# Optimization experiments

Measured on AMD Instinct MI355X. Metric: run time of the kernel, lower is better.

The kernel has to match this reference:

```python
import jax, jax.numpy as jnp
import numpy as np

N = 100_000      # total nodes in batched graph
NE = 800_000     # total edges
G = 1_000        # number of graphs in batch
V_DIM = 128      # node feat dim (== H_DIM, required by GRUCell usage)
E_DIM = 64       # edge feat dim
H_DIM = 128      # hidden dim
K_HEAD = 4       # multi-scale interaction heads


def _leaky(x):
    return jnp.where(x >= 0, x, 0.1 * x)


def _gru_cell(x, h, Wih, Whh, bih, bhh):
    # torch nn.GRUCell math; Wih/Whh stored as [in, 3*h] with (r,z,n) chunk order
    gi = x @ Wih + bih
    gh = h @ Whh + bhh
    ir, iz, inn = jnp.split(gi, 3, axis=-1)
    hr, hz, hn = jnp.split(gh, 3, axis=-1)
    r = jax.nn.sigmoid(ir + hr)
    z = jax.nn.sigmoid(iz + hz)
    n = jnp.tanh(inn + r * hn)
    return (1.0 - z) * n + z * h


def setup_inputs() -> dict:
    key = jax.random.key(0)
    ks = iter(jax.random.split(key, 48))
    def rn(shape, scale=0.05):
        return (jax.random.normal(next(ks), shape) * scale).astype(jnp.float32)
    inp = {}
    inp["v"] = rn((N, V_DIM), 1.0)
    inp["e"] = rn((NE, E_DIM), 1.0)
    inp["s"] = rn((G, V_DIM), 1.0)
    inp["edge_src"] = jax.random.randint(next(ks), (NE,), 0, N)
    inp["edge_dst"] = jax.random.randint(next(ks), (NE,), 0, N)
    inp["node_graph"] = jnp.repeat(jnp.arange(G), N // G)  # sorted segment ids
    # top-level linears (stored [in, out])
    inp["A_w"] = rn((V_DIM, H_DIM)); inp["A_b"] = rn((H_DIM,))
    inp["mA_w"] = rn((K_HEAD, V_DIM, H_DIM)); inp["mA_b"] = rn((K_HEAD, H_DIM))
    inp["mB_w"] = rn((K_HEAD, V_DIM, H_DIM)); inp["mB_b"] = rn((K_HEAD, H_DIM))
    inp["mC_w"] = rn((K_HEAD, H_DIM)); inp["mC_b"] = rn((K_HEAD,))
    inp["mD_w"] = rn((K_HEAD, V_DIM, H_DIM)); inp["mD_b"] = rn((K_HEAD, H_DIM))
    inp["B_w"] = rn((H_DIM * K_HEAD, H_DIM)); inp["B_b"] = rn((H_DIM,))
    inp["C_w"] = rn((V_DIM, H_DIM)); inp["C_b"] = rn((H_DIM,))
    inp["K_w"] = rn((E_DIM, H_DIM)); inp["K_b"] = rn((H_DIM,))
    inp["E_w"] = rn((H_DIM + V_DIM, H_DIM)); inp["E_b"] = rn((H_DIM,))
    for pfx in ("gm", "gs"):
        inp[pfx + "_A_w"] = rn((H_DIM, H_DIM)); inp[pfx + "_A_b"] = rn((H_DIM,))
        inp[pfx + "_B_w"] = rn((H_DIM, H_DIM)); inp[pfx + "_B_b"] = rn((H_DIM,))
        inp[pfx + "_Wih"] = rn((H_DIM, 3 * H_DIM)); inp[pfx + "_Whh"] = rn((H_DIM, 3 * H_DIM))
        inp[pfx + "_bih"] = rn((3 * H_DIM,)); inp[pfx + "_bhh"] = rn((3 * H_DIM,))
    return inp


def reference(v, e, s, edge_src, edge_dst, node_graph,
              A_w, A_b, mA_w, mA_b, mB_w, mB_b, mC_w, mC_b, mD_w, mD_b,
              B_w, B_b, C_w, C_b, K_w, K_b, E_w, E_b,
              gm_A_w, gm_A_b, gm_B_w, gm_B_b, gm_Wih, gm_Whh, gm_bih, gm_bhh,
              gs_A_w, gs_A_b, gs_B_w, gs_B_b, gs_Wih, gs_Whh, gs_bih, gs_bhh):
    # super -> super
    s2s = jnp.tanh(s @ A_w + A_b)                                       # [G,H]
    # multi-head node->super attention pooling (Multi_scale_interaction)
    d_node = jnp.tanh(jnp.einsum('nv,kvh->knh', v, mA_w) + mA_b[:, None, :])     # [K,N,H]
    d_super = jnp.tanh(jnp.einsum('gv,kvh->kgh', s, mB_w) + mB_b[:, None, :])    # [K,G,H]
    a = jnp.einsum('knh,kh->nk', d_node * d_super[:, node_graph, :], mC_w) + mC_b[None, :]  # [N,K]
    a_max = jax.ops.segment_max(a, node_graph, num_segments=G, indices_are_sorted=True)
    a_exp = jnp.exp(a - a_max[node_graph])
    denom = jax.ops.segment_sum(a_exp, node_graph, num_segments=G, indices_are_sorted=True)
    attn = a_exp / denom[node_graph]                                    # per-graph softmax, [N,K]
    d_v = jnp.einsum('nv,kvh->nkh', v, mD_w) + mD_b[None, :, :]         # [N,K,H]
    pooled = jax.ops.segment_sum(d_v * attn[:, :, None], node_graph, num_segments=G,
                                 indices_are_sorted=True)               # [G,K,H]
    m2s = jnp.tanh(pooled.reshape(G, K_HEAD * H_DIM) @ B_w + B_b)       # [G,H]
    # super -> node broadcast
    s2m = jnp.tanh(s @ C_w + C_b)[node_graph]                           # [N,H]
    # edge-wise message: leaky_relu(K(e) * v_src) summed into destination node
    ve = _leaky((e @ K_w + K_b) * v[edge_src])                          # [E,H]
    sve = jax.ops.segment_sum(ve, edge_dst, num_segments=N)             # [N,H]
    m2m = _leaky(jnp.concatenate([sve, v], axis=1) @ E_w + E_b)         # [N,H]
    # adaptive GRU gate: node update
    z_m = jax.nn.sigmoid(m2m @ gm_A_w + gm_A_b + s2m @ gm_B_w + gm_B_b)
    h_m = z_m * s2m + (1.0 - z_m) * m2m
    update_v = _gru_cell(v, h_m, gm_Wih, gm_Whh, gm_bih, gm_bhh)
    # adaptive GRU gate: supernode update
    z_s = jax.nn.sigmoid(s2s @ gs_A_w + gs_A_b + m2s @ gs_B_w + gs_B_b)
    h_s = z_s * m2s + (1.0 - z_s) * s2s
    update_s = _gru_cell(s, h_s, gs_Wih, gs_Whh, gs_bih, gs_bhh)
    return (update_v, update_s)
```

## Files before the change

### kernel.cpp

```cpp
#include <hip/hip_runtime.h>

#define NN   100000
#define NEDG 800000
#define NG   1000
#define HD   128
#define EDIM 64

typedef unsigned short u16;
typedef __bf16 bf16x8 __attribute__((ext_vector_type(8)));
typedef float f32x4 __attribute__((ext_vector_type(4)));
typedef u16 u16x8 __attribute__((ext_vector_type(8)));

#define MFMA16(a, b, c) __builtin_amdgcn_mfma_f32_16x16x32_bf16(a, b, c, 0, 0, 0)

#define WS_E    0
#define WS_GA   4096
#define WS_WIH  6144
#define WS_WHH  12288
#define WS_MA0  18432
#define WS_KW   26624
#define WS_LANES 27648

#define BF(base, NTT, ks, nt, lane) \
    (*(const bf16x8*)(wsw + (size_t)((base) + (((ks) * (NTT) + (nt)) * 64 + (lane))) * 8))

__device__ __forceinline__ float sigmoidf_(float x) { return 1.0f / (1.0f + __expf(-x)); }
__device__ __forceinline__ float tanhf_(float x) {
    float ax = fabsf(x);
    float e  = __expf(-2.0f * ax);
    float t  = (1.0f - e) / (1.0f + e);
    return copysignf(t, x);
}
__device__ __forceinline__ float leaky_(float x) { return x >= 0.f ? x : 0.1f * x; }
__device__ __forceinline__ u16 f2bf(float x) {
    union { float f; unsigned u; } c; c.f = x;
    unsigned r = c.u + 0x7FFF + ((c.u >> 16) & 1);
    return (u16)(r >> 16);
}
__device__ __forceinline__ float bfbits2f(unsigned hw) {
    union { unsigned u; float f; } c; c.u = hw << 16; return c.f;
}

__device__ __forceinline__ void stg4(u16* lds, int P, int r, int c0, float4 v4) {
    int byteoff = (c0 << 1) ^ ((r & 7) << 4);
    u16* p = lds + r * P + (byteoff >> 1);
    p[0] = f2bf(v4.x); p[1] = f2bf(v4.y); p[2] = f2bf(v4.z); p[3] = f2bf(v4.w);
}
__device__ __forceinline__ void stg1(u16* lds, int P, int r, int c, u16 val) {
    int byteoff = (c << 1) ^ ((r & 7) << 4);
    lds[r * P + (byteoff >> 1)] = val;
}
__device__ __forceinline__ bf16x8 ldA(const u16* lds, int P, int r, int ks, int hi) {
    int byteoff = (ks * 64 + (hi << 4)) ^ ((r & 7) << 4);
    return *(const bf16x8*)(lds + r * P + (byteoff >> 1));
}

__global__ __launch_bounds__(256) void wconv(
    const float* __restrict__ E_w, const float* __restrict__ gmA_w,
    const float* __restrict__ Wih, const float* __restrict__ Whh,
    const float* __restrict__ mA_w, const float* __restrict__ K_w,
    u16* __restrict__ dst)
{
    int t = blockIdx.x * 256 + threadIdx.x;
    if (t >= WS_LANES) return;
    const float* W; int N; int local;
    if (t < 4096)       { W = E_w;  N = 128; local = t; }
    else if (t < 6144)  { W = gmA_w; N = 128; local = t - 4096; }
    else if (t < 12288) { W = Wih;  N = 384; local = t - 6144; }
    else if (t < 18432) { W = Whh;  N = 384; local = t - 12288; }
    else if (t < 26624) { int k = (t - 18432) >> 11; W = mA_w + k * 128 * 128; N = 128; local = (t - 18432) & 2047; }
    else                { W = K_w;  N = 128; local = t - 26624; }
    int lane = local & 63;
    int fid  = local >> 6;
    int NT = N >> 4;
    int ks = fid / NT, nt = fid - ks * NT;
    int krow = ks * 32 + ((lane >> 4) << 3);
    int col  = nt * 16 + (lane & 15);
    u16* d = dst + (size_t)t * 8;
    #pragma unroll
    for (int j = 0; j < 8; j++) d[j] = f2bf(W[(size_t)(krow + j) * N + col]);
}

__global__ __launch_bounds__(256) void k_hist(const int* __restrict__ edst, int* __restrict__ cnt) {
    int i = blockIdx.x * 256 + threadIdx.x;
    if (i < NEDG) atomicAdd(&cnt[edst[i]], 1);
}

__global__ __launch_bounds__(256) void k_scan1(const int* __restrict__ cnt,
                                               int* __restrict__ excl, int* __restrict__ bsum) {
    __shared__ int sd[256];
    int t = threadIdx.x, b = blockIdx.x;
    int base = b * 1024 + t * 4;
    int v0 = (base + 0 < NN) ? cnt[base + 0] : 0;
    int v1 = (base + 1 < NN) ? cnt[base + 1] : 0;
    int v2 = (base + 2 < NN) ? cnt[base + 2] : 0;
    int v3 = (base + 3 < NN) ? cnt[base + 3] : 0;
    int s = v0 + v1 + v2 + v3;
    sd[t] = s;
    __syncthreads();
    for (int off = 1; off < 256; off <<= 1) {
        int x = (t >= off) ? sd[t - off] : 0;
        __syncthreads();
        sd[t] += x;
        __syncthreads();
    }
    int incl = sd[t];
    int ex = incl - s;
    if (base + 0 < NN) excl[base + 0] = ex;
    if (base + 1 < NN) excl[base + 1] = ex + v0;
    if (base + 2 < NN) excl[base + 2] = ex + v0 + v1;
    if (base + 3 < NN) excl[base + 3] = ex + v0 + v1 + v2;
    if (t == 255) bsum[b] = incl;
}

#define NSCB 98
__global__ void k_scan2(int* __restrict__ bsum) {
    if (threadIdx.x == 0 && blockIdx.x == 0) {
        int run = 0;
        for (int i = 0; i < NSCB; i++) { int t = bsum[i]; bsum[i] = run; run += t; }
    }
}

__global__ __launch_bounds__(256) void k_scan3(const int* __restrict__ excl,
                                               const int* __restrict__ bsum,
                                               int* __restrict__ start, int* __restrict__ rowptr) {
    int i = blockIdx.x * 256 + threadIdx.x;
    if (i < NN) {
        int sv = excl[i] + bsum[i >> 10];
        start[i] = sv;
        rowptr[i] = sv;
    }
    if (i == NN) rowptr[NN] = NEDG;
}

__global__ __launch_bounds__(256) void k_scatter(const int* __restrict__ edst,
                                                 int* __restrict__ start,
                                                 int* __restrict__ perm,
                                                 int* __restrict__ outpos) {
    int i = blockIdx.x * 256 + threadIdx.x;
    if (i < NEDG) {
        int pos = atomicAdd(&start[edst[i]], 1);
        perm[pos] = i;
        outpos[i] = pos;
    }
}

__global__ __launch_bounds__(128) void k1_graph(
    const float* __restrict__ s,
    const float* __restrict__ A_w, const float* __restrict__ A_b,
    const float* __restrict__ mB_w, const float* __restrict__ mB_b,
    const float* __restrict__ mC_w,
    const float* __restrict__ C_w, const float* __restrict__ C_b,
    const float* __restrict__ gmB_w, const float* __restrict__ gmA_b, const float* __restrict__ gmB_b,
    float* __restrict__ s2s, float* __restrict__ wkg,
    float* __restrict__ s2m_tab, float* __restrict__ t2)
{
    __shared__ float sm[HD];
    __shared__ float sm2[HD];
    const int g = blockIdx.x, t = threadIdx.x;
    sm[t] = s[g * HD + t];
    __syncthreads();
    {
        float a = 0.f;
        #pragma unroll 8
        for (int i = 0; i < HD; i++) a = fmaf(sm[i], A_w[i * HD + t], a);
        s2s[g * HD + t] = tanhf_(a + A_b[t]);
    }
    for (int k = 0; k < 4; k++) {
        float a = 0.f;
        const float* W = mB_w + k * HD * HD;
        #pragma unroll 8
        for (int i = 0; i < HD; i++) a = fmaf(sm[i], W[i * HD + t], a);
        float d = tanhf_(a + mB_b[k * HD + t]);
        wkg[(k * NG + g) * HD + t] = d * mC_w[k * HD + t];
    }
    float s2m;
    {
        float a = 0.f;
        #pragma unroll 8
        for (int i = 0; i < HD; i++) a = fmaf(sm[i], C_w[i * HD + t], a);
        s2m = tanhf_(a + C_b[t]);
        s2m_tab[g * HD + t] = s2m;
    }
    sm2[t] = s2m;
    __syncthreads();
    {
        float a = 0.f;
        #pragma unroll 8
        for (int i = 0; i < HD; i++) a = fmaf(sm2[i], gmB_w[i * HD + t], a);
        t2[g * HD + t] = a + gmA_b[t] + gmB_b[t];
    }
}

__global__ __launch_bounds__(256) void k2_ascore(
    const float* __restrict__ v, const int* __restrict__ ngr,
    const u16* __restrict__ wsw,
    const float* __restrict__ mA_b, const float* __restrict__ mC_b,
    const float* __restrict__ wkg,
    float* __restrict__ aexp, float* __restrict__ denom)
{
    __shared__ u16 VT[64 * 128];
    const int tid = threadIdx.x;
    const int n0 = blockIdx.x * 64;
    #pragma unroll
    for (int l = 0; l < 8; l++) {
        int i = tid + 256 * l;
        int r = i >> 5, c0 = (i & 31) << 2;
        int node = n0 + r;
        float4 vv = (node < NN) ? *(const float4*)(v + (size_t)node * HD + c0)
                                : make_float4(0.f, 0.f, 0.f, 0.f);
        stg4(VT, 128, r, c0, vv);
    }
    __syncthreads();
    const int lane = tid & 63, w = tid >> 6;
    const int l15 = lane & 15, hi = lane >> 4;
    const int rbase = w * 16;
    bf16x8 av[4];
    #pragma unroll
    for (int ks = 0; ks < 4; ks++) av[ks] = ldA(VT, 128, rbase + l15, ks, hi);
    int gq[4], nodeq[4];
    #pragma unroll
    for (int q = 0; q < 4; q++) {
        int nd = n0 + rbase + hi * 4 + q;
        nodeq[q] = nd;
        gq[q] = ngr[min(nd, NN - 1)];
    }
    for (int k = 0; k < 4; k++) {
        float rs[4] = {0.f, 0.f, 0.f, 0.f};
        const float* bias = mA_b + k * HD;
        #pragma unroll
        for (int nt = 0; nt < 8; nt++) {
            f32x4 acc = {0.f, 0.f, 0.f, 0.f};
            #pragma unroll
            for (int ks = 0; ks < 4; ks++)
                acc = MFMA16(av[ks], BF(WS_MA0 + k * 2048, 8, ks, nt, lane), acc);
            int col = nt * 16 + l15;
            float bb = bias[col];
            #pragma unroll
            for (int q = 0; q < 4; q++)
                rs[q] += tanhf_(acc[q] + bb) * wkg[((size_t)k * NG + gq[q]) * HD + col];
        }
        #pragma unroll
        for (int q = 0; q < 4; q++) {
            float x = rs[q];
            x += __shfl_xor(x, 1); x += __shfl_xor(x, 2);
            x += __shfl_xor(x, 4); x += __shfl_xor(x, 8);
            if (l15 == 0 && nodeq[q] < NN) {
                float ev = __expf(x + mC_b[k]);
                aexp[(size_t)nodeq[q] * 4 + k] = ev;
                atomicAdd(&denom[gq[q] * 4 + k], ev);
            }
        }
    }
}

__global__ __launch_bounds__(256) void k3a_edge(
    const float* __restrict__ e, const float* __restrict__ v,
    const int* __restrict__ esrc, const int* __restrict__ outpos,
    const u16* __restrict__ wsw, const float* __restrict__ K_b,
    u16* __restrict__ vesrt)
{
    __shared__ u16 ET[64 * 64];
    __shared__ u16 OUT[64 * 128];
    __shared__ int posa[64];
    const int tid = threadIdx.x;
    const int e0 = blockIdx.x * 64;
    if (tid < 64) posa[tid] = outpos[e0 + tid];
    #pragma unroll
    for (int l = 0; l < 4; l++) {
        int i = tid + 256 * l;
        int r = i >> 4, c0 = (i & 15) << 2;
        float4 ev4 = *(const float4*)(e + (size_t)(e0 + r) * EDIM + c0);
        stg4(ET, 64, r, c0, ev4);
    }
    __syncthreads();
    const int lane = tid & 63, w = tid >> 6;
    const int l15 = lane & 15, hi = lane >> 4;
    const int rbase = w * 16;
    bf16x8 ae[2];
    #pragma unroll
    for (int ks = 0; ks < 2; ks++) ae[ks] = ldA(ET, 64, rbase + l15, ks, hi);
    int sq[4];
    #pragma unroll
    for (int q = 0; q < 4; q++) sq[q] = esrc[e0 + rbase + hi * 4 + q];
    #pragma unroll
    for (int nt = 0; nt < 8; nt++) {
        f32x4 acc = {0.f, 0.f, 0.f, 0.f};
        acc = MFMA16(ae[0], BF(WS_KW, 8, 0, nt, lane), acc);
        acc = MFMA16(ae[1], BF(WS_KW, 8, 1, nt, lane), acc);
        int col = nt * 16 + l15;
        float kb = K_b[col];
        #pragma unroll
        for (int q = 0; q < 4; q++) {
            float val = leaky_((acc[q] + kb) * v[(size_t)sq[q] * HD + col]);
            stg1(OUT, 128, rbase + hi * 4 + q, col, f2bf(val));
        }
    }
    __syncthreads();
    #pragma unroll
    for (int l = 0; l < 4; l++) {
        int i = tid + 256 * l;
        int r = i >> 4, seg = i & 15;
        int segp = seg ^ (r & 7);
        u16x8 val = *(const u16x8*)&OUT[r * 128 + segp * 8];
        *(u16x8*)(vesrt + (size_t)posa[r] * HD + ((segp ^ (r & 7)) * 8)) = val;
    }
}

__global__ __launch_bounds__(256) void k3b_segsum(
    const u16* __restrict__ vesrt, const int* __restrict__ rowptr,
    float* __restrict__ sve)
{
    const int wid = threadIdx.x >> 6, lane = threadIdx.x & 63;
    const int n = blockIdx.x * 4 + wid;
    if (n >= NN) return;
    const int r0 = rowptr[n], r1 = rowptr[n + 1];
    const unsigned* base = (const unsigned*)vesrt;
    float a0 = 0.f, a1 = 0.f;
    int r = r0;
    for (; r + 4 <= r1; r += 4) {
        unsigned x0 = base[(size_t)(r + 0) * 64 + lane];
        unsigned x1 = base[(size_t)(r + 1) * 64 + lane];
        unsigned x2 = base[(size_t)(r + 2) * 64 + lane];
        unsigned x3 = base[(size_t)(r + 3) * 64 + lane];
        a0 += bfbits2f(x0 & 0xffff) + bfbits2f(x1 & 0xffff) + bfbits2f(x2 & 0xffff) + bfbits2f(x3 & 0xffff);
        a1 += bfbits2f(x0 >> 16) + bfbits2f(x1 >> 16) + bfbits2f(x2 >> 16) + bfbits2f(x3 >> 16);
    }
    for (; r < r1; r++) {
        unsigned x = base[(size_t)r * 64 + lane];
        a0 += bfbits2f(x & 0xffff);
        a1 += bfbits2f(x >> 16);
    }
    *(float2*)(sve + (size_t)n * HD + lane * 2) = make_float2(a0, a1);
}

__global__ __launch_bounds__(256) void k3_edge_sorted(
    const float* __restrict__ e, const float* __restrict__ v,
    const int* __restrict__ esrc, const int* __restrict__ edst,
    const int* __restrict__ perm,
    const u16* __restrict__ wsw, const float* __restrict__ K_b,
    float* __restrict__ sve)
{
    __shared__ u16 ET[64 * 64];
    __shared__ int pid[64];
    const int tid = threadIdx.x;
    const int e0 = blockIdx.x * 64;
    if (tid < 64) pid[tid] = perm[e0 + tid];
    __syncthreads();
    #pragma unroll
    for (int l = 0; l < 4; l++) {
        int i = tid + 256 * l;
        int r = i >> 4, c0 = (i & 15) << 2;
        float4 ev4 = *(const float4*)(e + (size_t)pid[r] * EDIM + c0);
        stg4(ET, 64, r, c0, ev4);
    }
    __syncthreads();
    const int lane = tid & 63, w = tid >> 6;
    const int l15 = lane & 15, hi = lane >> 4;
    const int rbase = w * 16;
    bf16x8 ae[2];
    #pragma unroll
    for (int ks = 0; ks < 2; ks++) ae[ks] = ldA(ET, 64, rbase + l15, ks, hi);
    int sq[4], dq[4];
    #pragma unroll
    for (int q = 0; q < 4; q++) {
        int ei = pid[rbase + hi * 4 + q];
        sq[q] = esrc[ei]; dq[q] = edst[ei];
    }
    #pragma unroll
    for (int nt = 0; nt < 8; nt++) {
        f32x4 acc = {0.f, 0.f, 0.f, 0.f};
        acc = MFMA16(ae[0], BF(WS_KW, 8, 0, nt, lane), acc);
        acc = MFMA16(ae[1], BF(WS_KW, 8, 1, nt, lane), acc);
        int col = nt * 16 + l15;
        float kb = K_b[col];
        float vals[4];
        #pragma unroll
        for (int q = 0; q < 4; q++)
            vals[q] = leaky_((acc[q] + kb) * v[(size_t)sq[q] * HD + col]);
        float a = vals[0];
        #pragma unroll
        for (int q = 1; q < 4; q++) {
            if (dq[q] == dq[q - 1]) a += vals[q];
            else { atomicAdd(&sve[(size_t)dq[q - 1] * HD + col], a); a = vals[q]; }
        }
        atomicAdd(&sve[(size_t)dq[3] * HD + col], a);
    }
}

__global__ __launch_bounds__(256) void k3_edge_unsorted(
    const float* __restrict__ e, const float* __restrict__ v,
    const int* __restrict__ esrc, const int* __restrict__ edst,
    const u16* __restrict__ wsw, const float* __restrict__ K_b,
    float* __restrict__ sve)
{
    __shared__ u16 ET[64 * 64];
    const int tid = threadIdx.x;
    const int e0 = blockIdx.x * 64;
    #pragma unroll
    for (int l = 0; l < 4; l++) {
        int i = tid + 256 * l;
        int r = i >> 4, c0 = (i & 15) << 2;
        float4 ev4 = *(const float4*)(e + (size_t)(e0 + r) * EDIM + c0);
        stg4(ET, 64, r, c0, ev4);
    }
    __syncthreads();
    const int lane = tid & 63, w = tid >> 6;
    const int l15 = lane & 15, hi = lane >> 4;
    const int rbase = w * 16;
    bf16x8 ae[2];
    #pragma unroll
    for (int ks = 0; ks < 2; ks++) ae[ks] = ldA(ET, 64, rbase + l15, ks, hi);
    int sq[4], dq[4];
    #pragma unroll
    for (int q = 0; q < 4; q++) {
        int ei = e0 + rbase + hi * 4 + q;
        sq[q] = esrc[ei]; dq[q] = edst[ei];
    }
    #pragma unroll
    for (int nt = 0; nt < 8; nt++) {
        f32x4 acc = {0.f, 0.f, 0.f, 0.f};
        acc = MFMA16(ae[0], BF(WS_KW, 8, 0, nt, lane), acc);
        acc = MFMA16(ae[1], BF(WS_KW, 8, 1, nt, lane), acc);
        int col = nt * 16 + l15;
        float kb = K_b[col];
        #pragma unroll
        for (int q = 0; q < 4; q++) {
            float val = leaky_((acc[q] + kb) * v[(size_t)sq[q] * HD + col]);
            atomicAdd(&sve[(size_t)dq[q] * HD + col], val);
        }
    }
}

__global__ __launch_bounds__(256) void k4_vbar(
    const float* __restrict__ v, const int* __restrict__ ngr,
    const float* __restrict__ aexp, const float* __restrict__ denom,
    float* __restrict__ vbar)
{
    const int tid = threadIdx.x;
    const int d = tid & 127;
    const int hf = tid >> 7;
    const int n0 = blockIdx.x * 32 + hf * 16;
    int gcur = -1;
    float a0 = 0.f, a1 = 0.f, a2 = 0.f, a3 = 0.f;
    float4 rd = make_float4(0.f, 0.f, 0.f, 0.f);
    for (int nd = 0; nd < 16; nd++) {
        int n = n0 + nd;
        int g = ngr[n];
        if (g != gcur) {
            if (gcur >= 0) {
                atomicAdd(&vbar[(gcur * 4 + 0) * HD + d], a0);
                atomicAdd(&vbar[(gcur * 4 + 1) * HD + d], a1);
                atomicAdd(&vbar[(gcur * 4 + 2) * HD + d], a2);
                atomicAdd(&vbar[(gcur * 4 + 3) * HD + d], a3);
                a0 = a1 = a2 = a3 = 0.f;
            }
            float4 dn = *(const float4*)&denom[g * 4];
            rd = make_float4(1.f / dn.x, 1.f / dn.y, 1.f / dn.z, 1.f / dn.w);
            gcur = g;
        }
        float4 ae = *(const float4*)&aexp[n * 4];
        float vv = v[(size_t)n * HD + d];
        a0 = fmaf(ae.x * rd.x, vv, a0);
        a1 = fmaf(ae.y * rd.y, vv, a1);
        a2 = fmaf(ae.z * rd.z, vv, a2);
        a3 = fmaf(ae.w * rd.w, vv, a3);
    }
    atomicAdd(&vbar[(gcur * 4 + 0) * HD + d], a0);
    atomicAdd(&vbar[(gcur * 4 + 1) * HD + d], a1);
    atomicAdd(&vbar[(gcur * 4 + 2) * HD + d], a2);
    atomicAdd(&vbar[(gcur * 4 + 3) * HD + d], a3);
}

__global__ __launch_bounds__(128) void k5_super(
    const float* __restrict__ s, const float* __restrict__ vbar,
    const float* __restrict__ mD_w, const float* __restrict__ mD_b,
    const float* __restrict__ B_w, const float* __restrict__ B_b,
    const float* __restrict__ s2s,
    const float* __restrict__ gsA_w, const float* __restrict__ gsA_b,
    const float* __restrict__ gsB_w, const float* __restrict__ gsB_b,
    const float* __restrict__ gsWih, const float* __restrict__ gsWhh,
    const float* __restrict__ gsbih, const float* __restrict__ gsbhh,
    float* __restrict__ out_s)
{
    __shared__ float vb[4 * HD];
    __shared__ float p[4 * HD];
    __shared__ float m2s_l[HD];
    __shared__ float s2s_l[HD];
    __shared__ float hs_l[HD];
    __shared__ float srow[HD];
    const int g = blockIdx.x, t = threadIdx.x;
    #pragma unroll
    for (int l = 0; l < 4; l++) vb[t + HD * l] = vbar[(size_t)g * 4 * HD + t + HD * l];
    srow[t]  = s[g * HD + t];
    s2s_l[t] = s2s[g * HD + t];
    __syncthreads();
    for (int k = 0; k < 4; k++) {
        float a = 0.f;
        const float* W = mD_w + k * HD * HD;
        #pragma unroll 8
        for (int i = 0; i < HD; i++) a = fmaf(vb[k * HD + i], W[i * HD + t], a);
        p[k * HD + t] = a + mD_b[k * HD + t];
    }
    __syncthreads();
    float m2s;
    {
        float a = 0.f;
        #pragma unroll 8
        for (int j = 0; j < 4 * HD; j++) a = fmaf(p[j], B_w[j * HD + t], a);
        m2s = tanhf_(a + B_b[t]);
        m2s_l[t] = m2s;
    }
    __syncthreads();
    float hs;
    {
        float za = 0.f, zb = 0.f;
        #pragma unroll 8
        for (int i = 0; i < HD; i++) {
            za = fmaf(s2s_l[i], gsA_w[i * HD + t], za);
            zb = fmaf(m2s_l[i], gsB_w[i * HD + t], zb);
        }
        float z = sigmoidf_(za + gsA_b[t] + zb + gsB_b[t]);
        hs = z * m2s + (1.f - z) * s2s_l[t];
        hs_l[t] = hs;
    }
    __syncthreads();
    float gi0 = 0.f, gh0 = 0.f, gi1 = 0.f, gh1 = 0.f, gi2 = 0.f, gh2 = 0.f;
    #pragma unroll 4
    for (int i = 0; i < HD; i++) {
        float sv = srow[i], hv = hs_l[i];
        gi0 = fmaf(sv, gsWih[i * 384 + t], gi0);
        gh0 = fmaf(hv, gsWhh[i * 384 + t], gh0);
        gi1 = fmaf(sv, gsWih[i * 384 + 128 + t], gi1);
        gh1 = fmaf(hv, gsWhh[i * 384 + 128 + t], gh1);
        gi2 = fmaf(sv, gsWih[i * 384 + 256 + t], gi2);
        gh2 = fmaf(hv, gsWhh[i * 384 + 256 + t], gh2);
    }
    float r  = sigmoidf_(gi0 + gsbih[t] + gh0 + gsbhh[t]);
    float z2 = sigmoidf_(gi1 + gsbih[128 + t] + gh1 + gsbhh[128 + t]);
    float nn = tanhf_(gi2 + gsbih[256 + t] + r * (gh2 + gsbhh[256 + t]));
    out_s[g * HD + t] = (1.f - z2) * nn + z2 * hs;
}

__global__ __launch_bounds__(256) void k6_node(
    const float* __restrict__ v, const int* __restrict__ ngr,
    const float* __restrict__ sve, const u16* __restrict__ wsw,
    const float* __restrict__ E_b,
    const float* __restrict__ s2m_tab, const float* __restrict__ t2,
    const float* __restrict__ bih, const float* __restrict__ bhh,
    float* __restrict__ out_v)
{
    __shared__ u16 VT[64 * 128];
    __shared__ u16 ST[64 * 128];
    __shared__ u16 XT[64 * 128];
    const int tid = threadIdx.x;
    const int n0 = blockIdx.x * 64;
    #pragma unroll
    for (int l = 0; l < 8; l++) {
        int i = tid + 256 * l;
        int r = i >> 5, c0 = (i & 31) << 2;
        int node = n0 + r;
        float4 a = (node < NN) ? *(const float4*)(v   + (size_t)node * HD + c0) : make_float4(0.f, 0.f, 0.f, 0.f);
        float4 b = (node < NN) ? *(const float4*)(sve + (size_t)node * HD + c0) : make_float4(0.f, 0.f, 0.f, 0.f);
        stg4(VT, 128, r, c0, a);
        stg4(ST, 128, r, c0, b);
    }
    __syncthreads();
    const int lane = tid & 63, w = tid >> 6;
    const int l15 = lane & 15, hi = lane >> 4;
    const int rbase = w * 16;
    bf16x8 av[4], ax[4];
    #pragma unroll
    for (int ks = 0; ks < 4; ks++) {
        av[ks] = ldA(VT, 128, rbase + l15, ks, hi);
        ax[ks] = ldA(ST, 128, rbase + l15, ks, hi);
    }
    int gq[4], nodeq[4];
    #pragma unroll
    for (int q = 0; q < 4; q++) {
        int nd = n0 + rbase + hi * 4 + q;
        nodeq[q] = nd;
        gq[q] = ngr[min(nd, NN - 1)];
    }
    f32x4 hmf[8];
    #pragma unroll
    for (int nt = 0; nt < 8; nt++) {
        f32x4 acc = {0.f, 0.f, 0.f, 0.f};
        #pragma unroll
        for (int ks = 0; ks < 4; ks++) acc = MFMA16(ax[ks], BF(WS_E, 8, ks, nt, lane), acc);
        #pragma unroll
        for (int ks = 0; ks < 4; ks++) acc = MFMA16(av[ks], BF(WS_E, 8, 4 + ks, nt, lane), acc);
        int col = nt * 16 + l15;
        float eb = E_b[col];
        f32x4 m;
        #pragma unroll
        for (int q = 0; q < 4; q++) m[q] = leaky_(acc[q] + eb);
        hmf[nt] = m;
    }
    #pragma unroll
    for (int nt = 0; nt < 8; nt++) {
        int col = nt * 16 + l15;
        #pragma unroll
        for (int q = 0; q < 4; q++) stg1(ST, 128, rbase + hi * 4 + q, col, f2bf(hmf[nt][q]));
    }
    bf16x8 am[4];
    #pragma unroll
    for (int ks = 0; ks < 4; ks++) am[ks] = ldA(ST, 128, rbase + l15, ks, hi);
    #pragma unroll
    for (int nt = 0; nt < 8; nt++) {
        f32x4 acc = {0.f, 0.f, 0.f, 0.f};
        #pragma unroll
        for (int ks = 0; ks < 4; ks++) acc = MFMA16(am[ks], BF(WS_GA, 8, ks, nt, lane), acc);
        int col = nt * 16 + l15;
        #pragma unroll
        for (int q = 0; q < 4; q++) {
            int g = gq[q];
            float z  = sigmoidf_(acc[q] + t2[(size_t)g * HD + col]);
            float hm = z * s2m_tab[(size_t)g * HD + col] + (1.f - z) * hmf[nt][q];
            hmf[nt][q] = hm;
            stg1(XT, 128, rbase + hi * 4 + q, col, f2bf(hm));
        }
    }
    bf16x8 ah[4];
    #pragma unroll
    for (int ks = 0; ks < 4; ks++) ah[ks] = ldA(XT, 128, rbase + l15, ks, hi);
    #pragma unroll
    for (int nt = 0; nt < 8; nt++) {
        f32x4 air = {0.f,0.f,0.f,0.f}, aiz = {0.f,0.f,0.f,0.f}, ain = {0.f,0.f,0.f,0.f};
        f32x4 ahr = {0.f,0.f,0.f,0.f}, ahz = {0.f,0.f,0.f,0.f}, ahn = {0.f,0.f,0.f,0.f};
        #pragma unroll
        for (int ks = 0; ks < 4; ks++) {
            air = MFMA16(av[ks], BF(WS_WIH, 24, ks, nt,      lane), air);
            ahr = MFMA16(ah[ks], BF(WS_WHH, 24, ks, nt,      lane), ahr);
            aiz = MFMA16(av[ks], BF(WS_WIH, 24, ks, nt + 8,  lane), aiz);
            ahz = MFMA16(ah[ks], BF(WS_WHH, 24, ks, nt + 8,  lane), ahz);
            ain = MFMA16(av[ks], BF(WS_WIH, 24, ks, nt + 16, lane), ain);
            ahn = MFMA16(ah[ks], BF(WS_WHH, 24, ks, nt + 16, lane), ahn);
        }
        int col = nt * 16 + l15;
        float br  = bih[col] + bhh[col];
        float bz  = bih[HD + col] + bhh[HD + col];
        float bi3 = bih[2 * HD + col];
        float bh3 = bhh[2 * HD + col];
        #pragma unroll
        for (int q = 0; q < 4; q++) {
            float r   = sigmoidf_(air[q] + ahr[q] + br);
            float z   = sigmoidf_(aiz[q] + ahz[q] + bz);
            float nnv = tanhf_(ain[q] + bi3 + r * (ahn[q] + bh3));
            if (nodeq[q] < NN)
                out_v[(size_t)nodeq[q] * HD + col] = (1.f - z) * nnv + z * hmf[nt][q];
        }
    }
}

extern "C" void kernel_launch(void* const* d_in, const int* in_sizes, int n_in,
                              void* d_out, int out_size, void* d_ws, size_t ws_size,
                              hipStream_t stream)
{
    const float* v    = (const float*)d_in[0];
    const float* e    = (const float*)d_in[1];
    const float* s    = (const float*)d_in[2];
    const int*   esrc = (const int*)d_in[3];
    const int*   edst = (const int*)d_in[4];
    const int*   ngr  = (const int*)d_in[5];
    const float* A_w  = (const float*)d_in[6];
    const float* A_b  = (const float*)d_in[7];
    const float* mA_w = (const float*)d_in[8];
    const float* mA_b = (const float*)d_in[9];
    const float* mB_w = (const float*)d_in[10];
    const float* mB_b = (const float*)d_in[11];
    const float* mC_w = (const float*)d_in[12];
    const float* mC_b = (const float*)d_in[13];
    const float* mD_w = (const float*)d_in[14];
    const float* mD_b = (const float*)d_in[15];
    const float* B_w  = (const float*)d_in[16];
    const float* B_b  = (const float*)d_in[17];
    const float* C_w  = (const float*)d_in[18];
    const float* C_b  = (const float*)d_in[19];
    const float* K_w  = (const float*)d_in[20];
    const float* K_b  = (const float*)d_in[21];
    const float* E_w  = (const float*)d_in[22];
    const float* E_b  = (const float*)d_in[23];
    const float* gmA_w = (const float*)d_in[24];
    const float* gmA_b = (const float*)d_in[25];
    const float* gmB_w = (const float*)d_in[26];
    const float* gmB_b = (const float*)d_in[27];
    const float* gmWih = (const float*)d_in[28];
    const float* gmWhh = (const float*)d_in[29];
    const float* gmbih = (const float*)d_in[30];
    const float* gmbhh = (const float*)d_in[31];
    const float* gsA_w = (const float*)d_in[32];
    const float* gsA_b = (const float*)d_in[33];
    const float* gsB_w = (const float*)d_in[34];
    const float* gsB_b = (const float*)d_in[35];
    const float* gsWih = (const float*)d_in[36];
    const float* gsWhh = (const float*)d_in[37];
    const float* gsbih = (const float*)d_in[38];
    const float* gsbhh = (const float*)d_in[39];

    float* ws      = (float*)d_ws;
    float* sve     = ws;
    float* aexp    = sve + 12800000;
    float* denom   = aexp + 400000;
    float* wkg     = denom + 4000;
    float* s2s     = wkg + 512000;
    float* s2m_tab = s2s + 128000;
    float* t2      = s2m_tab + 128000;
    float* vbar    = t2 + 128000;
    u16*   wswz    = (u16*)(vbar + 512000);
    int*   isc     = (int*)(wswz + 221184);
    int*   cnt     = isc;
    int*   excl    = cnt + 100000;
    int*   bsum    = excl + 100000;
    int*   startp  = bsum + 128;
    int*   rowptr  = startp + 100000;
    int*   perm    = rowptr + 100032;
    int*   outpos  = perm + 800000;
    u16*   vesrt   = (u16*)(outpos + 800000);
    const size_t NEED_SORT = ((size_t)((int*)vesrt - (int*)d_ws)) * 4;
    const size_t NEED_FULL = NEED_SORT + (size_t)102400000 * 2;
    const bool do_sort = ws_size >= NEED_SORT;
    const bool do_full = ws_size >= NEED_FULL;

    hipMemsetAsync(denom, 0, (size_t)4000 * 4, stream);
    hipMemsetAsync(vbar, 0, (size_t)512000 * 4, stream);
    if (!do_full) hipMemsetAsync(sve, 0, (size_t)12800000 * 4, stream);

    float* out_v = (float*)d_out;
    float* out_s = out_v + (size_t)NN * HD;

    wconv<<<(WS_LANES + 255) / 256, 256, 0, stream>>>(E_w, gmA_w, gmWih, gmWhh, mA_w, K_w, wswz);
    k1_graph<<<NG, 128, 0, stream>>>(s, A_w, A_b, mB_w, mB_b, mC_w, C_w, C_b,
                                     gmB_w, gmA_b, gmB_b, s2s, wkg, s2m_tab, t2);
    if (do_sort) {
        hipMemsetAsync(cnt, 0, (size_t)100000 * 4, stream);
        k_hist<<<(NEDG + 255) / 256, 256, 0, stream>>>(edst, cnt);
        k_scan1<<<NSCB, 256, 0, stream>>>(cnt, excl, bsum);
        k_scan2<<<1, 64, 0, stream>>>(bsum);
        k_scan3<<<(NN + 256) / 256, 256, 0, stream>>>(excl, bsum, startp, rowptr);
        k_scatter<<<(NEDG + 255) / 256, 256, 0, stream>>>(edst, startp, perm, outpos);
    }
    k2_ascore<<<(NN + 63) / 64, 256, 0, stream>>>(v, ngr, wswz, mA_b, mC_b, wkg, aexp, denom);
    if (do_full) {
        k3a_edge<<<NEDG / 64, 256, 0, stream>>>(e, v, esrc, outpos, wswz, K_b, vesrt);
        k3b_segsum<<<(NN + 3) / 4, 256, 0, stream>>>(vesrt, rowptr, sve);
    } else if (do_sort) {
        k3_edge_sorted<<<NEDG / 64, 256, 0, stream>>>(e, v, esrc, edst, perm, wswz, K_b, sve);
    } else {
        k3_edge_unsorted<<<NEDG / 64, 256, 0, stream>>>(e, v, esrc, edst, wswz, K_b, sve);
    }
    k4_vbar<<<NN / 32, 256, 0, stream>>>(v, ngr, aexp, denom, vbar);
    k5_super<<<NG, 128, 0, stream>>>(s, vbar, mD_w, mD_b, B_w, B_b, s2s,
                                     gsA_w, gsA_b, gsB_w, gsB_b,
                                     gsWih, gsWhh, gsbih, gsbhh, out_s);
    k6_node<<<(NN + 63) / 64, 256, 0, stream>>>(v, ngr, sve, wswz, E_b, s2m_tab, t2,
                                                gmbih, gmbhh, out_v);
}
```

Before: 734.7 us.

## Swap MFMA operands to compute transposed tiles and drop LDS staging

The MFMA operands are swapped so each lane holds one node or edge row with 4 contiguous output columns. Inputs are loaded straight from global memory into bf16 fragments, and outputs are written as float4/u16x4 vectors. Shared-memory staging, the syncthreads barriers and the scalar LDS stores are removed. In the node kernel, the intermediate activations are redistributed between MFMA stages with cross-lane shuffles instead of an LDS round-trip. The trade-off is more shuffles and per-lane strided global reads of input rows that were previously coalesced through LDS.

```diff
diff --git a/kernel.cpp b/kernel.cpp
--- a/kernel.cpp
+++ b/kernel.cpp
@@ -9,7 +9,8 @@
 typedef unsigned short u16;
 typedef __bf16 bf16x8 __attribute__((ext_vector_type(8)));
 typedef float f32x4 __attribute__((ext_vector_type(4)));
-typedef u16 u16x8 __attribute__((ext_vector_type(8)));
+typedef u16 u16x4 __attribute__((ext_vector_type(4)));
+typedef unsigned u32x4 __attribute__((ext_vector_type(4)));
 
 #define MFMA16(a, b, c) __builtin_amdgcn_mfma_f32_16x16x32_bf16(a, b, c, 0, 0, 0)
 
@@ -40,15 +41,24 @@
 __device__ __forceinline__ float bfbits2f(unsigned hw) {
     union { unsigned u; float f; } c; c.u = hw << 16; return c.f;
 }
+__device__ __forceinline__ unsigned pack2bf(float lo, float hi) {
+    return (unsigned)f2bf(lo) | ((unsigned)f2bf(hi) << 16);
+}
+__device__ __forceinline__ bf16x8 mk8(const float* __restrict__ p) {
+    float4 a = *(const float4*)p;
+    float4 b = *(const float4*)(p + 4);
+    union { u32x4 u; bf16x8 v; } c;
+    c.u[0] = pack2bf(a.x, a.y);
+    c.u[1] = pack2bf(a.z, a.w);
+    c.u[2] = pack2bf(b.x, b.y);
+    c.u[3] = pack2bf(b.z, b.w);
+    return c.v;
+}
 
 __device__ __forceinline__ void stg4(u16* lds, int P, int r, int c0, float4 v4) {
     int byteoff = (c0 << 1) ^ ((r & 7) << 4);
     u16* p = lds + r * P + (byteoff >> 1);
     p[0] = f2bf(v4.x); p[1] = f2bf(v4.y); p[2] = f2bf(v4.z); p[3] = f2bf(v4.w);
-}
-__device__ __forceinline__ void stg1(u16* lds, int P, int r, int c, u16 val) {
-    int byteoff = (c << 1) ^ ((r & 7) << 4);
-    lds[r * P + (byteoff >> 1)] = val;
 }
 __device__ __forceinline__ bf16x8 ldA(const u16* lds, int P, int r, int ks, int hi) {
     int byteoff = (ks * 64 + (hi << 4)) ^ ((r & 7) << 4);
@@ -199,57 +209,37 @@
     const float* __restrict__ wkg,
     float* __restrict__ aexp, float* __restrict__ denom)
 {
-    __shared__ u16 VT[64 * 128];
     const int tid = threadIdx.x;
-    const int n0 = blockIdx.x * 64;
-    #pragma unroll
-    for (int l = 0; l < 8; l++) {
-        int i = tid + 256 * l;
-        int r = i >> 5, c0 = (i & 31) << 2;
-        int node = n0 + r;
-        float4 vv = (node < NN) ? *(const float4*)(v + (size_t)node * HD + c0)
-                                : make_float4(0.f, 0.f, 0.f, 0.f);
-        stg4(VT, 128, r, c0, vv);
-    }
-    __syncthreads();
     const int lane = tid & 63, w = tid >> 6;
-    const int l15 = lane & 15, hi = lane >> 4;
-    const int rbase = w * 16;
+    const int l15 = lane & 15, hi = lane >> 4, cb = hi * 4;
+    const int node = blockIdx.x * 64 + w * 16 + l15;
+    const int nodec = min(node, NN - 1);
+    const int g = ngr[nodec];
     bf16x8 av[4];
     #pragma unroll
-    for (int ks = 0; ks < 4; ks++) av[ks] = ldA(VT, 128, rbase + l15, ks, hi);
-    int gq[4], nodeq[4];
-    #pragma unroll
-    for (int q = 0; q < 4; q++) {
-        int nd = n0 + rbase + hi * 4 + q;
-        nodeq[q] = nd;
-        gq[q] = ngr[min(nd, NN - 1)];
-    }
+    for (int ks = 0; ks < 4; ks++) av[ks] = mk8(v + (size_t)nodec * HD + ks * 32 + hi * 8);
+    #pragma unroll
     for (int k = 0; k < 4; k++) {
-        float rs[4] = {0.f, 0.f, 0.f, 0.f};
+        float rs = 0.f;
         const float* bias = mA_b + k * HD;
+        const float* wrow = wkg + ((size_t)k * NG + g) * HD;
         #pragma unroll
         for (int nt = 0; nt < 8; nt++) {
             f32x4 acc = {0.f, 0.f, 0.f, 0.f};
             #pragma unroll
             for (int ks = 0; ks < 4; ks++)
-                acc = MFMA16(av[ks], BF(WS_MA0 + k * 2048, 8, ks, nt, lane), acc);
-            int col = nt * 16 + l15;
-            float bb = bias[col];
-            #pragma unroll
-            for (int q = 0; q < 4; q++)
-                rs[q] += tanhf_(acc[q] + bb) * wkg[((size_t)k * NG + gq[q]) * HD + col];
+                acc = MFMA16(BF(WS_MA0 + k * 2048, 8, ks, nt, lane), av[ks], acc);
+            float4 bb = *(const float4*)&bias[nt * 16 + cb];
+            float4 wk = *(const float4*)&wrow[nt * 16 + cb];
+            rs += tanhf_(acc[0] + bb.x) * wk.x + tanhf_(acc[1] + bb.y) * wk.y
+                + tanhf_(acc[2] + bb.z) * wk.z + tanhf_(acc[3] + bb.w) * wk.w;
         }
-        #pragma unroll
-        for (int q = 0; q < 4; q++) {
-            float x = rs[q];
-            x += __shfl_xor(x, 1); x += __shfl_xor(x, 2);
-            x += __shfl_xor(x, 4); x += __shfl_xor(x, 8);
-            if (l15 == 0 && nodeq[q] < NN) {
-                float ev = __expf(x + mC_b[k]);
-                aexp[(size_t)nodeq[q] * 4 + k] = ev;
-                atomicAdd(&denom[gq[q] * 4 + k], ev);
-            }
+        rs += __shfl_xor(rs, 16);
+        rs += __shfl_xor(rs, 32);
+        if (hi == 0 && node < NN) {
+            float ev = __expf(rs + mC_b[k]);
+            aexp[(size_t)node * 4 + k] = ev;
+            atomicAdd(&denom[g * 4 + k], ev);
         }
     }
 }
@@ -260,50 +250,29 @@
     const u16* __restrict__ wsw, const float* __restrict__ K_b,
     u16* __restrict__ vesrt)
 {
-    __shared__ u16 ET[64 * 64];
-    __shared__ u16 OUT[64 * 128];
-    __shared__ int posa[64];
     const int tid = threadIdx.x;
-    const int e0 = blockIdx.x * 64;
-    if (tid < 64) posa[tid] = outpos[e0 + tid];
-    #pragma unroll
-    for (int l = 0; l < 4; l++) {
-        int i = tid + 256 * l;
-        int r = i >> 4, c0 = (i & 15) << 2;
-        float4 ev4 = *(const float4*)(e + (size_t)(e0 + r) * EDIM + c0);
-        stg4(ET, 64, r, c0, ev4);
-    }
-    __syncthreads();
     const int lane = tid & 63, w = tid >> 6;
-    const int l15 = lane & 15, hi = lane >> 4;
-    const int rbase = w * 16;
-    bf16x8 ae[2];
-    #pragma unroll
-    for (int ks = 0; ks < 2; ks++) ae[ks] = ldA(ET, 64, rbase + l15, ks, hi);
-    int sq[4];
-    #pragma unroll
-    for (int q = 0; q < 4; q++) sq[q] = esrc[e0 + rbase + hi * 4 + q];
+    const int l15 = lane & 15, hi = lane >> 4, cb = hi * 4;
+    const int edge = blockIdx.x * 64 + w * 16 + l15;
+    const int sq = esrc[edge];
+    const int pos = outpos[edge];
+    bf16x8 ae0 = mk8(e + (size_t)edge * EDIM + hi * 8);
+    bf16x8 ae1 = mk8(e + (size_t)edge * EDIM + 32 + hi * 8);
+    const float* vrow = v + (size_t)sq * HD;
+    u16* drow = vesrt + (size_t)pos * HD;
     #pragma unroll
     for (int nt = 0; nt < 8; nt++) {
         f32x4 acc = {0.f, 0.f, 0.f, 0.f};
-        acc = MFMA16(ae[0], BF(WS_KW, 8, 0, nt, lane), acc);
-        acc = MFMA16(ae[1], BF(WS_KW, 8, 1, nt, lane), acc);
-        int col = nt * 16 + l15;
-        float kb = K_b[col];
-        #pragma unroll
-        for (int q = 0; q < 4; q++) {
-            float val = leaky_((acc[q] + kb) * v[(size_t)sq[q] * HD + col]);
-            stg1(OUT, 128, rbase + hi * 4 + q, col, f2bf(val));
-        }
-    }
-    __syncthreads();
-    #pragma unroll
-    for (int l = 0; l < 4; l++) {
-        int i = tid + 256 * l;
-        int r = i >> 4, seg = i & 15;
-        int segp = seg ^ (r & 7);
-        u16x8 val = *(const u16x8*)&OUT[r * 128 + segp * 8];
-        *(u16x8*)(vesrt + (size_t)posa[r] * HD + ((segp ^ (r & 7)) * 8)) = val;
+        acc = MFMA16(BF(WS_KW, 8, 0, nt, lane), ae0, acc);
+        acc = MFMA16(BF(WS_KW, 8, 1, nt, lane), ae1, acc);
+        float4 kb = *(const float4*)&K_b[nt * 16 + cb];
+        float4 vv = *(const float4*)&vrow[nt * 16 + cb];
+        u16x4 o;
+        o[0] = f2bf(leaky_((acc[0] + kb.x) * vv.x));
+        o[1] = f2bf(leaky_((acc[1] + kb.y) * vv.y));
+        o[2] = f2bf(leaky_((acc[2] + kb.z) * vv.z));
+        o[3] = f2bf(leaky_((acc[3] + kb.w) * vv.w));
+        *(u16x4*)(drow + nt * 16 + cb) = o;
     }
 }
 
@@ -550,106 +519,143 @@
     const float* __restrict__ bih, const float* __restrict__ bhh,
     float* __restrict__ out_v)
 {
-    __shared__ u16 VT[64 * 128];
-    __shared__ u16 ST[64 * 128];
-    __shared__ u16 XT[64 * 128];
     const int tid = threadIdx.x;
-    const int n0 = blockIdx.x * 64;
-    #pragma unroll
-    for (int l = 0; l < 8; l++) {
-        int i = tid + 256 * l;
-        int r = i >> 5, c0 = (i & 31) << 2;
-        int node = n0 + r;
-        float4 a = (node < NN) ? *(const float4*)(v   + (size_t)node * HD + c0) : make_float4(0.f, 0.f, 0.f, 0.f);
-        float4 b = (node < NN) ? *(const float4*)(sve + (size_t)node * HD + c0) : make_float4(0.f, 0.f, 0.f, 0.f);
-        stg4(VT, 128, r, c0, a);
-        stg4(ST, 128, r, c0, b);
-    }
-    __syncthreads();
     const int lane = tid & 63, w = tid >> 6;
-    const int l15 = lane & 15, hi = lane >> 4;
-    const int rbase = w * 16;
+    const int l15 = lane & 15, hi = lane >> 4, cb = hi * 4;
+    const int node = blockIdx.x * 64 + w * 16 + l15;
+    const int nodec = min(node, NN - 1);
+    const bool ok = node < NN;
+    const int g = ngr[nodec];
+    const int srcA = l15 + 32 * (hi & 1);
+    const int srcB = srcA + 16;
+    const bool sel = (hi >> 1) != 0;
+
     bf16x8 av[4], ax[4];
     #pragma unroll
     for (int ks = 0; ks < 4; ks++) {
-        av[ks] = ldA(VT, 128, rbase + l15, ks, hi);
-        ax[ks] = ldA(ST, 128, rbase + l15, ks, hi);
-    }
-    int gq[4], nodeq[4];
-    #pragma unroll
-    for (int q = 0; q < 4; q++) {
-        int nd = n0 + rbase + hi * 4 + q;
-        nodeq[q] = nd;
-        gq[q] = ngr[min(nd, NN - 1)];
-    }
-    f32x4 hmf[8];
+        av[ks] = mk8(v   + (size_t)nodec * HD + ks * 32 + hi * 8);
+        ax[ks] = mk8(sve + (size_t)nodec * HD + ks * 32 + hi * 8);
+    }
+    f32x4 m2m[8];
     #pragma unroll
     for (int nt = 0; nt < 8; nt++) {
         f32x4 acc = {0.f, 0.f, 0.f, 0.f};
         #pragma unroll
-        for (int ks = 0; ks < 4; ks++) acc = MFMA16(ax[ks], BF(WS_E, 8, ks, nt, lane), acc);
+        for (int ks = 0; ks < 4; ks++) acc = MFMA16(BF(WS_E, 8, ks, nt, lane), ax[ks], acc);
         #pragma unroll
-        for (int ks = 0; ks < 4; ks++) acc = MFMA16(av[ks], BF(WS_E, 8, 4 + ks, nt, lane), acc);
-        int col = nt * 16 + l15;
-        float eb = E_b[col];
-        f32x4 m;
-        #pragma unroll
-        for (int q = 0; q < 4; q++) m[q] = leaky_(acc[q] + eb);
-        hmf[nt] = m;
-    }
+        for (int ks = 0; ks < 4; ks++) acc = MFMA16(BF(WS_E, 8, 4 + ks, nt, lane), av[ks], acc);
+        float4 eb = *(const float4*)&E_b[nt * 16 + cb];
+        m2m[nt][0] = leaky_(acc[0] + eb.x);
+        m2m[nt][1] = leaky_(acc[1] + eb.y);
+        m2m[nt][2] = leaky_(acc[2] + eb.z);
+        m2m[nt][3] = leaky_(acc[3] + eb.w);
+    }
+    unsigned pk[8][2];
     #pragma unroll
     for (int nt = 0; nt < 8; nt++) {
-        int col = nt * 16 + l15;
-        #pragma unroll
-        for (int q = 0; q < 4; q++) stg1(ST, 128, rbase + hi * 4 + q, col, f2bf(hmf[nt][q]));
-    }
-    bf16x8 am[4];
-    #pragma unroll
-    for (int ks = 0; ks < 4; ks++) am[ks] = ldA(ST, 128, rbase + l15, ks, hi);
+        pk[nt][0] = pack2bf(m2m[nt][0], m2m[nt][1]);
+        pk[nt][1] = pack2bf(m2m[nt][2], m2m[nt][3]);
+    }
+    bf16x8 bm[4];
+    #pragma unroll
+    for (int ks = 0; ks < 4; ks++) {
+        unsigned a0 = (unsigned)__shfl((int)pk[2 * ks][0],     srcA);
+        unsigned a1 = (unsigned)__shfl((int)pk[2 * ks][1],     srcA);
+        unsigned b0 = (unsigned)__shfl((int)pk[2 * ks + 1][0], srcA);
+        unsigned b1 = (unsigned)__shfl((int)pk[2 * ks + 1][1], srcA);
+        unsigned c0 = (unsigned)__shfl((int)pk[2 * ks][0],     srcB);
+        unsigned c1 = (unsigned)__shfl((int)pk[2 * ks][1],     srcB);
+        unsigned d0 = (unsigned)__shfl((int)pk[2 * ks + 1][0], srcB);
+        unsigned d1 = (unsigned)__shfl((int)pk[2 * ks + 1][1], srcB);
+        union { u32x4 u; bf16x8 b; } c;
+        c.u[0] = sel ? b0 : a0;
+        c.u[1] = sel ? b1 : a1;
+        c.u[2] = sel ? d0 : c0;
+        c.u[3] = sel ? d1 : c1;
+        bm[ks] = c.b;
+    }
+    const float* t2row = t2 + (size_t)g * HD;
+    const float* s2row = s2m_tab + (size_t)g * HD;
+    f32x4 hm[8];
     #pragma unroll
     for (int nt = 0; nt < 8; nt++) {
         f32x4 acc = {0.f, 0.f, 0.f, 0.f};
         #pragma unroll
-        for (int ks = 0; ks < 4; ks++) acc = MFMA16(am[ks], BF(WS_GA, 8, ks, nt, lane), acc);
-        int col = nt * 16 + l15;
-        #pragma unroll
-        for (int q = 0; q < 4; q++) {
-            int g = gq[q];
-            float z  = sigmoidf_(acc[q] + t2[(size_t)g * HD + col]);
-            float hm = z * s2m_tab[(size_t)g * HD + col] + (1.f - z) * hmf[nt][q];
-            hmf[nt][q] = hm;
-            stg1(XT, 128, rbase + hi * 4 + q, col, f2bf(hm));
-        }
-    }
-    bf16x8 ah[4];
-    #pragma unroll
-    for (int ks = 0; ks < 4; ks++) ah[ks] = ldA(XT, 128, rbase + l15, ks, hi);
+        for (int ks = 0; ks < 4; ks++) acc = MFMA16(BF(WS_GA, 8, ks, nt, lane), bm[ks], acc);
+        float4 t2v = *(const float4*)&t2row[nt * 16 + cb];
+        float4 s2v = *(const float4*)&s2row[nt * 16 + cb];
+        float z0 = sigmoidf_(acc[0] + t2v.x);
+        float z1 = sigmoidf_(acc[1] + t2v.y);
+        float z2 = sigmoidf_(acc[2] + t2v.z);
+        float z3 = sigmoidf_(acc[3] + t2v.w);
+        hm[nt][0] = z0 * s2v.x + (1.f - z0) * m2m[nt][0];
+        hm[nt][1] = z1 * s2v.y + (1.f - z1) * m2m[nt][1];
+        hm[nt][2] = z2 * s2v.z + (1.f - z2) * m2m[nt][2];
+        hm[nt][3] = z3 * s2v.w + (1.f - z3) * m2m[nt][3];
+    }
+    #pragma unroll
+    for (int nt = 0; nt < 8; nt++) {
+        pk[nt][0] = pack2bf(hm[nt][0], hm[nt][1]);
+        pk[nt][1] = pack2bf(hm[nt][2], hm[nt][3]);
+    }
+    bf16x8 bh[4];
+    #pragma unroll
+    for (int ks = 0; ks < 4; ks++) {
+        unsigned a0 = (unsigned)__shfl((int)pk[2 * ks][0],     srcA);
+        unsigned a1 = (unsigned)__shfl((int)pk[2 * ks][1],     srcA);
+        unsigned b0 = (unsigned)__shfl((int)pk[2 * ks + 1][0], srcA);
+        unsigned b1 = (unsigned)__shfl((int)pk[2 * ks + 1][1], srcA);
+        unsigned c0 = (unsigned)__shfl((int)pk[2 * ks][0],     srcB);
+        unsigned c1 = (unsigned)__shfl((int)pk[2 * ks][1],     srcB);
+        unsigned d0 = (unsigned)__shfl((int)pk[2 * ks + 1][0], srcB);
+        unsigned d1 = (unsigned)__shfl((int)pk[2 * ks + 1][1], srcB);
+        union { u32x4 u; bf16x8 b; } c;
+        c.u[0] = sel ? b0 : a0;
+        c.u[1] = sel ? b1 : a1;
+        c.u[2] = sel ? d0 : c0;
+        c.u[3] = sel ? d1 : c1;
+        bh[ks] = c.b;
+    }
+    float* orow = out_v + (size_t)node * HD;
     #pragma unroll
     for (int nt = 0; nt < 8; nt++) {
         f32x4 air = {0.f,0.f,0.f,0.f}, aiz = {0.f,0.f,0.f,0.f}, ain = {0.f,0.f,0.f,0.f};
         f32x4 ahr = {0.f,0.f,0.f,0.f}, ahz = {0.f,0.f,0.f,0.f}, ahn = {0.f,0.f,0.f,0.f};
         #pragma unroll
         for (int ks = 0; ks < 4; ks++) {
-            air = MFMA16(av[ks], BF(WS_WIH, 24, ks, nt,      lane), air);
-            ahr = MFMA16(ah[ks], BF(WS_WHH, 24, ks, nt,      lane), ahr);
-            aiz = MFMA16(av[ks], BF(WS_WIH, 24, ks, nt + 8,  lane), aiz);
-            ahz = MFMA16(ah[ks], BF(WS_WHH, 24, ks, nt + 8,  lane), ahz);
-            ain = MFMA16(av[ks], BF(WS_WIH, 24, ks, nt + 16, lane), ain);
-            ahn = MFMA16(ah[ks], BF(WS_WHH, 24, ks, nt + 16, lane), ahn);
+            air = MFMA16(BF(WS_WIH, 24, ks, nt,      lane), av[ks], air);
+            ahr = MFMA16(BF(WS_WHH, 24, ks, nt,      lane), bh[ks], ahr);
+            aiz = MFMA16(BF(WS_WIH, 24, ks, nt + 8,  lane), av[ks], aiz);
+            ahz = MFMA16(BF(WS_WHH, 24, ks, nt + 8,  lane), bh[ks], ahz);
+            ain = MFMA16(BF(WS_WIH, 24, ks, nt + 16, lane), av[ks], ain);
+            ahn = MFMA16(BF(WS_WHH, 24, ks, nt + 16, lane), bh[ks], ahn);
         }
-        int col = nt * 16 + l15;
-        float br  = bih[col] + bhh[col];
-        float bz  = bih[HD + col] + bhh[HD + col];
-        float bi3 = bih[2 * HD + col];
-        float bh3 = bhh[2 * HD + col];
-        #pragma unroll
-        for (int q = 0; q < 4; q++) {
-            float r   = sigmoidf_(air[q] + ahr[q] + br);
-            float z   = sigmoidf_(aiz[q] + ahz[q] + bz);
-            float nnv = tanhf_(ain[q] + bi3 + r * (ahn[q] + bh3));
-            if (nodeq[q] < NN)
-                out_v[(size_t)nodeq[q] * HD + col] = (1.f - z) * nnv + z * hmf[nt][q];
+        float4 bir = *(const float4*)&bih[nt * 16 + cb];
+        float4 bhr = *(const float4*)&bhh[nt * 16 + cb];
+        float4 biz = *(const float4*)&bih[HD + nt * 16 + cb];
+        float4 bhz = *(const float4*)&bhh[HD + nt * 16 + cb];
+        float4 bin = *(const float4*)&bih[2 * HD + nt * 16 + cb];
+        float4 bhn = *(const float4*)&bhh[2 * HD + nt * 16 + cb];
+        float4 outv;
+        {
+            float r0 = sigmoidf_(air[0] + ahr[0] + bir.x + bhr.x);
+            float z0 = sigmoidf_(aiz[0] + ahz[0] + biz.x + bhz.x);
+            float n0 = tanhf_(ain[0] + bin.x + r0 * (ahn[0] + bhn.x));
+            outv.x = (1.f - z0) * n0 + z0 * hm[nt][0];
+            float r1 = sigmoidf_(air[1] + ahr[1] + bir.y + bhr.y);
+            float z1 = sigmoidf_(aiz[1] + ahz[1] + biz.y + bhz.y);
+            float n1 = tanhf_(ain[1] + bin.y + r1 * (ahn[1] + bhn.y));
+            outv.y = (1.f - z1) * n1 + z1 * hm[nt][1];
+            float r2 = sigmoidf_(air[2] + ahr[2] + bir.z + bhr.z);
+            float z2 = sigmoidf_(aiz[2] + ahz[2] + biz.z + bhz.z);
+            float n2 = tanhf_(ain[2] + bin.z + r2 * (ahn[2] + bhn.z));
+            outv.z = (1.f - z2) * n2 + z2 * hm[nt][2];
+            float r3 = sigmoidf_(air[3] + ahr[3] + bir.w + bhr.w);
+            float z3 = sigmoidf_(aiz[3] + ahz[3] + biz.w + bhz.w);
+            float n3 = tanhf_(ain[3] + bin.w + r3 * (ahn[3] + bhn.w));
+            outv.w = (1.f - z3) * n3 + z3 * hm[nt][3];
         }
+        if (ok) *(float4*)(orow + nt * 16 + cb) = outv;
     }
 }
 
```

Measured after the change: 832.5 us. 13.3% more time.
